# Kernel tuning notes

Hardware: AMD Instinct MI355X
Metric: run time of the kernel (lower is better)

Reference implementation:

```python
import jax, jax.numpy as jnp
import numpy as np

T, H, I, E, TOPK = 4096, 2880, 2880, 16, 4
EPS = 1e-5
ALPHA = 1.702


def setup_inputs() -> dict:
    key = jax.random.key(0)
    ks = jax.random.split(key, 8)
    s = 0.02
    return {
        "x": jax.random.normal(ks[0], (T, H), dtype=jnp.float32),
        "norm_w": jnp.ones((H,), dtype=jnp.float32),
        "gate_w": jax.random.normal(ks[1], (E, H), dtype=jnp.float32) * s,
        "gate_b": jax.random.normal(ks[2], (E,), dtype=jnp.float32) * s,
        "w1": jax.random.normal(ks[3], (E, 2 * I, H), dtype=jnp.float32) * s,  # fused gate_up
        "b1": jax.random.normal(ks[4], (E, 2 * I), dtype=jnp.float32) * s,
        "w2": jax.random.normal(ks[5], (E, H, I), dtype=jnp.float32) * s,      # down proj
        "b2": jax.random.normal(ks[6], (E, H), dtype=jnp.float32) * s,
    }


def _rmsnorm(x, w, eps=EPS):
    var = jnp.mean(x * x, axis=-1, keepdims=True)
    return x * jax.lax.rsqrt(var + eps) * w


def _swiglu(gu):
    glu, lin = jnp.split(gu, 2, axis=-1)
    return glu * jax.nn.sigmoid(ALPHA * glu) * (lin + 1.0)


def reference(x, norm_w, gate_w, gate_b, w1, b1, w2, b2):
    t = _rmsnorm(x, norm_w)                       # [T, H]
    logits = t @ gate_w.T + gate_b                # [T, E]
    # Renormalize routing: top-k of logits, softmax over the k selected logits
    vals, idx = jax.lax.top_k(logits, TOPK)       # [T, k]
    wts = jax.nn.softmax(vals, axis=-1)           # [T, k]
    combine = jnp.zeros((t.shape[0], E), dtype=t.dtype)
    combine = combine.at[jnp.arange(t.shape[0])[:, None], idx].set(wts)  # [T, E]
    out = jnp.zeros_like(x)
    for e in range(E):                            # small fixed expert loop
        gu = t @ w1[e].T + b1[e]                  # [T, 2I]
        y = _swiglu(gu) @ w2[e].T + b2[e]         # [T, H]
        out = out + combine[:, e:e + 1] * y
    return x + out
```

## Files before the change

kernel.cpp:

```cpp
#include <hip/hip_runtime.h>
#include <hip/hip_bf16.h>
#include <math.h>
#include <stdint.h>

#define T_TOK 4096
#define H_DIM 2880
#define E_NUM 16
#define ALPHA 1.702f
#define EPS_RMS 1e-5f

#define PADM 192
#define BK 32
#define NK (H_DIM / BK)
#define MAX_RT 104
#define NCT1 30
#define NCT2 15
#define G1 (MAX_RT * NCT1)
#define G2 (MAX_RT * NCT2)
#define ABUF 12288
#define BBUF 12288
#define BOFF 36864

typedef __attribute__((ext_vector_type(8))) short short8;
typedef __attribute__((ext_vector_type(4))) float f32x4;

__device__ __forceinline__ unsigned short f2bf(float f) {
  unsigned u = __float_as_uint(f);
  return (unsigned short)((u + 0x7fffu + ((u >> 16) & 1u)) >> 16);
}
__device__ __forceinline__ unsigned cpk(float a, float b) {
  unsigned r;
  asm("v_cvt_pk_bf16_f32 %0, %1, %2" : "=v"(r) : "v"(a), "v"(b));
  return r;
}
__device__ __forceinline__ void gl_lds16(const void* g, unsigned char* lds_dst) {
  __builtin_amdgcn_global_load_lds(
      (const __attribute__((address_space(1))) void*)g,
      (__attribute__((address_space(3))) void*)lds_dst, 16, 0, 0);
}
#define ENDSTEP() do {                                           \
    asm volatile("s_waitcnt lgkmcnt(0)" ::: "memory");           \
    __builtin_amdgcn_s_barrier();                                \
    __builtin_amdgcn_sched_barrier(0);                           \
  } while (0)

__global__ __launch_bounds__(256) void k_norm_gate(
    const float* __restrict__ x, const float* __restrict__ norm_w,
    const float* __restrict__ gate_w, const float* __restrict__ gate_b,
    unsigned short* __restrict__ t_out,
    int* __restrict__ topk_id, float* __restrict__ topk_w,
    int* __restrict__ counts)
{
  int t = blockIdx.x, tid = threadIdx.x;
  const float4* xr = (const float4*)(x + (size_t)t * H_DIM);
  float4 xa[3];
  float ss = 0.f;
  int j = 0;
  for (int i = tid; i < 720; i += 256, j++) {
    float4 v = xr[i]; xa[j] = v;
    ss += v.x * v.x + v.y * v.y + v.z * v.z + v.w * v.w;
  }
#pragma unroll
  for (int o = 1; o < 64; o <<= 1) ss += __shfl_xor(ss, o, 64);
  __shared__ float red[4];
  if ((tid & 63) == 0) red[tid >> 6] = ss;
  __syncthreads();
  float rs = rsqrtf((red[0] + red[1] + red[2] + red[3]) * (1.f / H_DIM) + EPS_RMS);

  float part[16];
#pragma unroll
  for (int q = 0; q < 16; q++) part[q] = 0.f;
  j = 0;
  for (int i = tid; i < 720; i += 256, j++) {
    float4 v = xa[j];
    float4 w = ((const float4*)norm_w)[i];
    float t0 = v.x * rs * w.x, t1 = v.y * rs * w.y;
    float t2 = v.z * rs * w.z, t3 = v.w * rs * w.w;
    ushort4 b; b.x = f2bf(t0); b.y = f2bf(t1); b.z = f2bf(t2); b.w = f2bf(t3);
    ((ushort4*)(t_out + (size_t)t * H_DIM))[i] = b;
#pragma unroll
    for (int q = 0; q < 16; q++) {
      float4 g = ((const float4*)(gate_w + (size_t)q * H_DIM))[i];
      part[q] += t0 * g.x + t1 * g.y + t2 * g.z + t3 * g.w;
    }
  }
  __shared__ float lg[4][16];
#pragma unroll
  for (int q = 0; q < 16; q++) {
    float p = part[q];
#pragma unroll
    for (int o = 1; o < 64; o <<= 1) p += __shfl_xor(p, o, 64);
    if ((tid & 63) == 0) lg[tid >> 6][q] = p;
  }
  __syncthreads();
  if (tid == 0) {
    float logit[16];
    for (int q = 0; q < 16; q++)
      logit[q] = lg[0][q] + lg[1][q] + lg[2][q] + lg[3][q] + gate_b[q];
    unsigned used = 0; int idx[4]; float val[4];
    for (int k = 0; k < 4; k++) {
      float best = -3.4e38f; int bi = 0;
      for (int q = 0; q < 16; q++)
        if (!((used >> q) & 1u) && logit[q] > best) { best = logit[q]; bi = q; }
      used |= 1u << bi; idx[k] = bi; val[k] = best;
    }
    float s0 = 0.f, w4[4];
    for (int k = 0; k < 4; k++) { w4[k] = expf(val[k] - val[0]); s0 += w4[k]; }
    for (int k = 0; k < 4; k++) {
      topk_id[t * 4 + k] = idx[k];
      topk_w[t * 4 + k] = w4[k] / s0;
      atomicAdd(&counts[idx[k]], 1);
    }
  }
}

__global__ void k_offsets(const int* __restrict__ counts, int* __restrict__ d_off) {
  if (threadIdx.x == 0) {
    int acc = 0;
    for (int q = 0; q < 16; q++) {
      d_off[q] = acc;
      acc += ((counts[q] + PADM - 1) / PADM) * PADM;
    }
    d_off[16] = acc;
  }
}

__global__ __launch_bounds__(256) void k_fill(
    const int* __restrict__ topk_id, const float* __restrict__ topk_w,
    const int* __restrict__ counts, const int* __restrict__ d_off,
    int* __restrict__ perm_tok, float* __restrict__ perm_w,
    int* __restrict__ perm_sl)
{
  int e = blockIdx.x;
  int base = d_off[e], pe = d_off[e + 1] - base, cnt = counts[e];
  int tid = threadIdx.x, lane = tid & 63, wv = tid >> 6;
  __shared__ int wsum[4];
  int pos = 0;
  for (int c0 = 0; c0 < T_TOK; c0 += 256) {
    int tok = c0 + tid;
    int4 ids = ((const int4*)topk_id)[tok];
    int flag = 0, slot = 0;
    if (ids.x == e) { flag = 1; slot = 0; }
    else if (ids.y == e) { flag = 1; slot = 1; }
    else if (ids.z == e) { flag = 1; slot = 2; }
    else if (ids.w == e) { flag = 1; slot = 3; }
    unsigned long long b = __ballot(flag);
    int wprefix = __popcll(b & ((1ULL << lane) - 1ULL));
    if (lane == 0) wsum[wv] = __popcll(b);
    __syncthreads();
    int woff = 0;
    for (int i = 0; i < wv; i++) woff += wsum[i];
    int tot = wsum[0] + wsum[1] + wsum[2] + wsum[3];
    if (flag) {
      int p = base + pos + woff + wprefix;
      perm_tok[p] = tok;
      perm_w[p] = topk_w[tok * 4 + slot];
      perm_sl[p] = slot;
    }
    pos += tot;
    __syncthreads();
  }
  for (int i = cnt + tid; i < pe; i += 256) {
    perm_tok[base + i] = -1;
    perm_w[base + i] = 0.f;
    perm_sl[base + i] = 0;
  }
}

#define STAGE_A(abuf, ktn) do {                                               \
  gl_lds16(aptr0 + (size_t)(ktn) * BK, lds + (abuf) * ABUF + adst0);          \
  if (tid < 256)                                                              \
    gl_lds16(aptr1 + (size_t)(ktn) * BK, lds + (abuf) * ABUF + adst1);        \
} while (0)

#define LOAD_B(ktn) do {                                                      \
  bv[0][0] = bptr0[(ktn) * 8]; bv[0][1] = bptr0[(ktn) * 8 + 1];               \
  if (tid < 256) { bv[1][0] = bptr1[(ktn) * 8]; bv[1][1] = bptr1[(ktn) * 8 + 1]; } \
} while (0)

#define PACK_B(bbuf) do {                                                     \
  uint4 p0;                                                                   \
  p0.x = cpk(bv[0][0].x, bv[0][0].y); p0.y = cpk(bv[0][0].z, bv[0][0].w);     \
  p0.z = cpk(bv[0][1].x, bv[0][1].y); p0.w = cpk(bv[0][1].z, bv[0][1].w);     \
  *(uint4*)(lds + BOFF + (bbuf) * BBUF + bdst0) = p0;                         \
  if (tid < 256) {                                                            \
    uint4 p1;                                                                 \
    p1.x = cpk(bv[1][0].x, bv[1][0].y); p1.y = cpk(bv[1][0].z, bv[1][0].w);   \
    p1.z = cpk(bv[1][1].x, bv[1][1].y); p1.w = cpk(bv[1][1].z, bv[1][1].w);   \
    *(uint4*)(lds + BOFF + (bbuf) * BBUF + bdst1) = p1;                       \
  }                                                                           \
} while (0)

#define GEMM_PIPE(COMP) do {                                                  \
  STAGE_A(0, 0); STAGE_A(1, 1); LOAD_B(0);                                    \
  PACK_B(0);                                                                  \
  ENDSTEP();                                                                  \
  int ca = 0;                                                                 \
  _Pragma("unroll 1")                                                         \
  for (int u = 0; u < NK / 2; u++) {                                          \
    int kt = 2 * u;                                                           \
    int ca1 = ca + 1; if (ca1 >= 3) ca1 -= 3;                                 \
    int ca2 = ca + 2; if (ca2 >= 3) ca2 -= 3;                                 \
    if (kt + 1 < NK) LOAD_B(kt + 1);                                          \
    if (kt + 2 < NK) STAGE_A(ca2, kt + 2);                                    \
    COMP(ca, 0);                                                              \
    if (kt + 1 < NK) PACK_B(1);                                               \
    ENDSTEP();                                                                \
    if (kt + 2 < NK) LOAD_B(kt + 2);                                          \
    if (kt + 3 < NK) STAGE_A(ca, kt + 3);                                     \
    COMP(ca1, 1);                                                             \
    if (kt + 2 < NK) PACK_B(0);                                               \
    ENDSTEP();                                                                \
    ca = ca2;                                                                 \
  }                                                                           \
} while (0)

#define COMP1(ab, bb) do {                                                    \
  const unsigned char* Ab = lds + (ab) * ABUF;                                \
  const unsigned char* Bb = lds + BOFF + (bb) * BBUF;                         \
  short8 a0 = *(const short8*)(Ab + abase);                                   \
  short8 a1 = *(const short8*)(Ab + abase + 1024);                            \
  short8 a2 = *(const short8*)(Ab + abase + 2048);                            \
  __builtin_amdgcn_s_setprio(1);                                              \
  _Pragma("unroll")                                                           \
  for (int n = 0; n < 3; n++) {                                               \
    short8 bg = *(const short8*)(Bb + bgbase + n * 1024);                     \
    short8 bl = *(const short8*)(Bb + blbase + n * 1024);                     \
    accg[0][n] = __builtin_amdgcn_mfma_f32_16x16x32_bf16(a0, bg, accg[0][n], 0, 0, 0); \
    accg[1][n] = __builtin_amdgcn_mfma_f32_16x16x32_bf16(a1, bg, accg[1][n], 0, 0, 0); \
    accg[2][n] = __builtin_amdgcn_mfma_f32_16x16x32_bf16(a2, bg, accg[2][n], 0, 0, 0); \
    accl[0][n] = __builtin_amdgcn_mfma_f32_16x16x32_bf16(a0, bl, accl[0][n], 0, 0, 0); \
    accl[1][n] = __builtin_amdgcn_mfma_f32_16x16x32_bf16(a1, bl, accl[1][n], 0, 0, 0); \
    accl[2][n] = __builtin_amdgcn_mfma_f32_16x16x32_bf16(a2, bl, accl[2][n], 0, 0, 0); \
  }                                                                           \
  __builtin_amdgcn_s_setprio(0);                                              \
} while (0)

#define COMP2(ab, bb) do {                                                    \
  const unsigned char* Ab = lds + (ab) * ABUF;                                \
  const unsigned char* Bb = lds + BOFF + (bb) * BBUF;                         \
  short8 a0 = *(const short8*)(Ab + abase);                                   \
  short8 a1 = *(const short8*)(Ab + abase + 1024);                            \
  short8 a2 = *(const short8*)(Ab + abase + 2048);                            \
  __builtin_amdgcn_s_setprio(1);                                              \
  _Pragma("unroll")                                                           \
  for (int n = 0; n < 6; n++) {                                               \
    short8 b = *(const short8*)(Bb + bbase + n * 1024);                       \
    acc[0][n] = __builtin_amdgcn_mfma_f32_16x16x32_bf16(a0, b, acc[0][n], 0, 0, 0); \
    acc[1][n] = __builtin_amdgcn_mfma_f32_16x16x32_bf16(a1, b, acc[1][n], 0, 0, 0); \
    acc[2][n] = __builtin_amdgcn_mfma_f32_16x16x32_bf16(a2, b, acc[2][n], 0, 0, 0); \
  }                                                                           \
  __builtin_amdgcn_s_setprio(0);                                              \
} while (0)

__global__ __launch_bounds__(512, 4) void k_gemm1(
    const unsigned short* __restrict__ t_bf16,
    const float* __restrict__ w1, const float* __restrict__ b1,
    const int* __restrict__ perm_tok, const int* __restrict__ d_off,
    unsigned short* __restrict__ act)
{
  __shared__ __align__(16) unsigned char lds[3 * ABUF + 2 * BBUF];
  const int total = d_off[16];
  int bid = blockIdx.x;
  int wg = (bid & 7) * (G1 / 8) + (bid >> 3);
  int ct = wg / MAX_RT, rt = wg % MAX_RT;
  int rowbase = rt * PADM;
  if (rowbase >= total) return;
  int e = 0;
#pragma unroll
  for (int q = 0; q < E_NUM; q++) if (d_off[q + 1] <= rowbase) e = q + 1;

  int tid = threadIdx.x, lane = tid & 63, wv = tid >> 6;
  int wm = wv & 3, wn = wv >> 2;
  int lr = lane & 15, ch = lane >> 4;
  unsigned swz16 = (unsigned)((ch ^ ((lr >> 1) & 3)) << 4);
  unsigned abase  = (unsigned)((wm * 48 + lr) * 64) + swz16;
  unsigned bgbase = (unsigned)((wn * 48 + lr) * 64) + swz16;
  unsigned blbase = bgbase + 6144;

  const unsigned short* aptr0; const unsigned short* aptr1 = 0;
  unsigned adst0, adst1 = 0;
  {
    int cl = tid, r = cl >> 2, c = cl & 3;
    int tok = perm_tok[rowbase + r]; if (tok < 0) tok = 0;
    aptr0 = t_bf16 + (size_t)tok * H_DIM + ((c ^ ((r >> 1) & 3)) * 8);
    adst0 = (unsigned)cl * 16;
  }
  if (tid < 256) {
    int cl = 512 + tid, r = cl >> 2, c = cl & 3;
    int tok = perm_tok[rowbase + r]; if (tok < 0) tok = 0;
    aptr1 = t_bf16 + (size_t)tok * H_DIM + ((c ^ ((r >> 1) & 3)) * 8);
    adst1 = (unsigned)cl * 16;
  }
  const float4* bptr0; const float4* bptr1 = 0;
  unsigned bdst0, bdst1 = 0;
  {
    int cl = tid, rr = cl >> 2, c = cl & 3;
    size_t grow = (size_t)e * (2 * H_DIM) +
                  (rr < 96 ? (size_t)(ct * 96 + rr) : (size_t)(H_DIM + ct * 96 + (rr - 96)));
    bptr0 = (const float4*)(w1 + grow * H_DIM) + c * 2;
    bdst0 = (unsigned)(rr * 64 + ((c ^ ((rr >> 1) & 3)) << 4));
  }
  if (tid < 256) {
    int cl = 512 + tid, rr = cl >> 2, c = cl & 3;
    size_t grow = (size_t)(H_DIM + ct * 96 + (rr - 96)) + (size_t)e * (2 * H_DIM);
    bptr1 = (const float4*)(w1 + grow * H_DIM) + c * 2;
    bdst1 = (unsigned)(rr * 64 + ((c ^ ((rr >> 1) & 3)) << 4));
  }

  f32x4 zero = {0.f, 0.f, 0.f, 0.f};
  f32x4 accg[3][3], accl[3][3];
#pragma unroll
  for (int m = 0; m < 3; m++)
#pragma unroll
    for (int n = 0; n < 3; n++) { accg[m][n] = zero; accl[m][n] = zero; }
  float4 bv[2][2];

  GEMM_PIPE(COMP1);

  int rq = lane >> 4;
#pragma unroll
  for (int m = 0; m < 3; m++) {
    int row0 = rowbase + wm * 48 + m * 16 + rq * 4;
#pragma unroll
    for (int n = 0; n < 3; n++) {
      int col = ct * 96 + wn * 48 + n * 16 + lr;
      float bg = b1[(size_t)e * (2 * H_DIM) + col];
      float bl = b1[(size_t)e * (2 * H_DIM) + H_DIM + col];
#pragma unroll
      for (int j = 0; j < 4; j++) {
        float g = accg[m][n][j] + bg;
        float l = accl[m][n][j] + bl;
        float s = 1.f / (1.f + __expf(-ALPHA * g));
        act[(size_t)(row0 + j) * H_DIM + col] = f2bf(g * s * (l + 1.f));
      }
    }
  }
}

__global__ __launch_bounds__(512, 4) void k_gemm2(
    const unsigned short* __restrict__ act,
    const float* __restrict__ w2, const float* __restrict__ b2,
    const int* __restrict__ perm_tok, const float* __restrict__ perm_w,
    const int* __restrict__ perm_sl, const int* __restrict__ d_off,
    unsigned short* __restrict__ yslot)
{
  __shared__ __align__(16) unsigned char lds[3 * ABUF + 2 * BBUF];
  __shared__ int stok[PADM]; __shared__ float swt[PADM]; __shared__ int ssl[PADM];
  const int total = d_off[16];
  int bid = blockIdx.x;
  int wg = (bid & 7) * (G2 / 8) + (bid >> 3);
  int ct = wg / MAX_RT, rt = wg % MAX_RT;
  int rowbase = rt * PADM;
  if (rowbase >= total) return;
  int e = 0;
#pragma unroll
  for (int q = 0; q < E_NUM; q++) if (d_off[q + 1] <= rowbase) e = q + 1;

  int tid = threadIdx.x, lane = tid & 63, wv = tid >> 6;
  int wm = wv & 3, wn = wv >> 2;
  int lr = lane & 15, ch = lane >> 4;
  unsigned swz16 = (unsigned)((ch ^ ((lr >> 1) & 3)) << 4);
  unsigned abase = (unsigned)((wm * 48 + lr) * 64) + swz16;
  unsigned bbase = (unsigned)((wn * 96 + lr) * 64) + swz16;

  if (tid < PADM) {
    stok[tid] = perm_tok[rowbase + tid];
    swt[tid] = perm_w[rowbase + tid];
    ssl[tid] = perm_sl[rowbase + tid];
  }

  const unsigned short* aptr0; const unsigned short* aptr1 = 0;
  unsigned adst0, adst1 = 0;
  {
    int cl = tid, r = cl >> 2, c = cl & 3;
    aptr0 = act + (size_t)(rowbase + r) * H_DIM + ((c ^ ((r >> 1) & 3)) * 8);
    adst0 = (unsigned)cl * 16;
  }
  if (tid < 256) {
    int cl = 512 + tid, r = cl >> 2, c = cl & 3;
    aptr1 = act + (size_t)(rowbase + r) * H_DIM + ((c ^ ((r >> 1) & 3)) * 8);
    adst1 = (unsigned)cl * 16;
  }
  const float4* bptr0; const float4* bptr1 = 0;
  unsigned bdst0, bdst1 = 0;
  {
    int cl = tid, rr = cl >> 2, c = cl & 3;
    size_t grow = (size_t)e * H_DIM + (size_t)(ct * 192 + rr);
    bptr0 = (const float4*)(w2 + grow * H_DIM) + c * 2;
    bdst0 = (unsigned)(rr * 64 + ((c ^ ((rr >> 1) & 3)) << 4));
  }
  if (tid < 256) {
    int cl = 512 + tid, rr = cl >> 2, c = cl & 3;
    size_t grow = (size_t)e * H_DIM + (size_t)(ct * 192 + rr);
    bptr1 = (const float4*)(w2 + grow * H_DIM) + c * 2;
    bdst1 = (unsigned)(rr * 64 + ((c ^ ((rr >> 1) & 3)) << 4));
  }

  f32x4 zero = {0.f, 0.f, 0.f, 0.f};
  f32x4 acc[3][6];
#pragma unroll
  for (int m = 0; m < 3; m++)
#pragma unroll
    for (int n = 0; n < 6; n++) acc[m][n] = zero;
  float4 bv[2][2];

  GEMM_PIPE(COMP2);

  int rq = lane >> 4;
#pragma unroll
  for (int m = 0; m < 3; m++) {
    int rl0 = wm * 48 + m * 16 + rq * 4;
#pragma unroll
    for (int n = 0; n < 6; n++) {
      int col = ct * 192 + wn * 96 + n * 16 + lr;
      float b2v = b2[(size_t)e * H_DIM + col];
#pragma unroll
      for (int j = 0; j < 4; j++) {
        int rl = rl0 + j;
        int tk = stok[rl];
        if (tk >= 0) {
          float y = (acc[m][n][j] + b2v) * swt[rl];
          yslot[((size_t)ssl[rl] * T_TOK + tk) * H_DIM + col] = f2bf(y);
        }
      }
    }
  }
}

__global__ __launch_bounds__(256) void k_comb(
    const float* __restrict__ x, const unsigned short* __restrict__ yslot,
    float* __restrict__ out)
{
  const int n8 = T_TOK * H_DIM / 8;
  int i = blockIdx.x * 256 + threadIdx.x;
  int stride = gridDim.x * 256;
  for (; i < n8; i += stride) {
    float4 x0 = ((const float4*)x)[2 * i];
    float4 x1 = ((const float4*)x)[2 * i + 1];
    float s[8] = {x0.x, x0.y, x0.z, x0.w, x1.x, x1.y, x1.z, x1.w};
#pragma unroll
    for (int k = 0; k < 4; k++) {
      uint4 v = ((const uint4*)(yslot + (size_t)k * T_TOK * H_DIM))[i];
      unsigned u[4] = {v.x, v.y, v.z, v.w};
#pragma unroll
      for (int q = 0; q < 4; q++) {
        s[2 * q]     += __uint_as_float(u[q] << 16);
        s[2 * q + 1] += __uint_as_float(u[q] & 0xffff0000u);
      }
    }
    float4 o0 = {s[0], s[1], s[2], s[3]};
    float4 o1 = {s[4], s[5], s[6], s[7]};
    ((float4*)out)[2 * i] = o0;
    ((float4*)out)[2 * i + 1] = o1;
  }
}

extern "C" void kernel_launch(void* const* d_in, const int* in_sizes, int n_in,
                              void* d_out, int out_size, void* d_ws, size_t ws_size,
                              hipStream_t stream)
{
  const float* x      = (const float*)d_in[0];
  const float* norm_w = (const float*)d_in[1];
  const float* gate_w = (const float*)d_in[2];
  const float* gate_b = (const float*)d_in[3];
  const float* w1     = (const float*)d_in[4];
  const float* b1     = (const float*)d_in[5];
  const float* w2     = (const float*)d_in[6];
  const float* b2     = (const float*)d_in[7];
  float* out = (float*)d_out;
  char* ws = (char*)d_ws;

  unsigned short* t_bf16  = (unsigned short*)(ws);
  unsigned short* act     = (unsigned short*)(ws + 23592960);
  int*            topk_id = (int*)(ws + 138608640);
  float*          topk_w  = (float*)(ws + 138674176);
  int*            perm_tk = (int*)(ws + 138739712);
  float*          perm_w  = (float*)(ws + 138819584);
  int*            perm_sl = (int*)(ws + 138899456);
  int*            counts  = (int*)(ws + 138979328);
  int*            d_off   = (int*)(ws + 138979392);
  unsigned short* yslot   = (unsigned short*)(ws + 138979840);

  hipMemsetAsync(counts, 0, 64, stream);
  hipLaunchKernelGGL(k_norm_gate, dim3(T_TOK), dim3(256), 0, stream,
                     x, norm_w, gate_w, gate_b, t_bf16, topk_id, topk_w, counts);
  hipLaunchKernelGGL(k_offsets, dim3(1), dim3(64), 0, stream, counts, d_off);
  hipLaunchKernelGGL(k_fill, dim3(16), dim3(256), 0, stream,
                     topk_id, topk_w, counts, d_off, perm_tk, perm_w, perm_sl);
  hipLaunchKernelGGL(k_gemm1, dim3(G1), dim3(512), 0, stream,
                     t_bf16, w1, b1, perm_tk, d_off, act);
  hipLaunchKernelGGL(k_gemm2, dim3(G2), dim3(512), 0, stream,
                     act, w2, b2, perm_tk, perm_w, perm_sl, d_off, yslot);
  hipLaunchKernelGGL(k_comb, dim3(2048), dim3(256), 0, stream, x, yslot, out);
}
```

Before: 1.484 ms.

## Load A fragments directly from global into registers, drop A LDS staging

```diff
diff --git a/kernel.cpp b/kernel.cpp
--- a/kernel.cpp
+++ b/kernel.cpp
@@ -17,9 +17,7 @@
 #define NCT2 15
 #define G1 (MAX_RT * NCT1)
 #define G2 (MAX_RT * NCT2)
-#define ABUF 12288
 #define BBUF 12288
-#define BOFF 36864
 
 typedef __attribute__((ext_vector_type(8))) short short8;
 typedef __attribute__((ext_vector_type(4))) float f32x4;
@@ -32,11 +30,6 @@
   unsigned r;
   asm("v_cvt_pk_bf16_f32 %0, %1, %2" : "=v"(r) : "v"(a), "v"(b));
   return r;
-}
-__device__ __forceinline__ void gl_lds16(const void* g, unsigned char* lds_dst) {
-  __builtin_amdgcn_global_load_lds(
-      (const __attribute__((address_space(1))) void*)g,
-      (__attribute__((address_space(3))) void*)lds_dst, 16, 0, 0);
 }
 #define ENDSTEP() do {                                           \
     asm volatile("s_waitcnt lgkmcnt(0)" ::: "memory");           \
@@ -167,10 +160,10 @@
   }
 }
 
-#define STAGE_A(abuf, ktn) do {                                               \
-  gl_lds16(aptr0 + (size_t)(ktn) * BK, lds + (abuf) * ABUF + adst0);          \
-  if (tid < 256)                                                              \
-    gl_lds16(aptr1 + (size_t)(ktn) * BK, lds + (abuf) * ABUF + adst1);        \
+#define LOAD_A(ar, ktn) do {                                                  \
+  ar[0] = *(const short8*)(aptrs[0] + (size_t)(ktn) * 64);                    \
+  ar[1] = *(const short8*)(aptrs[1] + (size_t)(ktn) * 64);                    \
+  ar[2] = *(const short8*)(aptrs[2] + (size_t)(ktn) * 64);                    \
 } while (0)
 
 #define LOAD_B(ktn) do {                                                      \
@@ -182,84 +175,71 @@
   uint4 p0;                                                                   \
   p0.x = cpk(bv[0][0].x, bv[0][0].y); p0.y = cpk(bv[0][0].z, bv[0][0].w);     \
   p0.z = cpk(bv[0][1].x, bv[0][1].y); p0.w = cpk(bv[0][1].z, bv[0][1].w);     \
-  *(uint4*)(lds + BOFF + (bbuf) * BBUF + bdst0) = p0;                         \
+  *(uint4*)(lds + (bbuf) * BBUF + bdst0) = p0;                                \
   if (tid < 256) {                                                            \
     uint4 p1;                                                                 \
     p1.x = cpk(bv[1][0].x, bv[1][0].y); p1.y = cpk(bv[1][0].z, bv[1][0].w);   \
     p1.z = cpk(bv[1][1].x, bv[1][1].y); p1.w = cpk(bv[1][1].z, bv[1][1].w);   \
-    *(uint4*)(lds + BOFF + (bbuf) * BBUF + bdst1) = p1;                       \
+    *(uint4*)(lds + (bbuf) * BBUF + bdst1) = p1;                              \
   }                                                                           \
 } while (0)
 
 #define GEMM_PIPE(COMP) do {                                                  \
-  STAGE_A(0, 0); STAGE_A(1, 1); LOAD_B(0);                                    \
+  LOAD_A(arA, 0);                                                             \
+  LOAD_B(0);                                                                  \
   PACK_B(0);                                                                  \
   ENDSTEP();                                                                  \
-  int ca = 0;                                                                 \
   _Pragma("unroll 1")                                                         \
   for (int u = 0; u < NK / 2; u++) {                                          \
     int kt = 2 * u;                                                           \
-    int ca1 = ca + 1; if (ca1 >= 3) ca1 -= 3;                                 \
-    int ca2 = ca + 2; if (ca2 >= 3) ca2 -= 3;                                 \
-    if (kt + 1 < NK) LOAD_B(kt + 1);                                          \
-    if (kt + 2 < NK) STAGE_A(ca2, kt + 2);                                    \
-    COMP(ca, 0);                                                              \
+    if (kt + 1 < NK) { LOAD_B(kt + 1); LOAD_A(arB, kt + 1); }                 \
+    COMP(arA, 0);                                                             \
     if (kt + 1 < NK) PACK_B(1);                                               \
     ENDSTEP();                                                                \
-    if (kt + 2 < NK) LOAD_B(kt + 2);                                          \
-    if (kt + 3 < NK) STAGE_A(ca, kt + 3);                                     \
-    COMP(ca1, 1);                                                             \
+    if (kt + 2 < NK) { LOAD_B(kt + 2); LOAD_A(arA, kt + 2); }                 \
+    COMP(arB, 1);                                                             \
     if (kt + 2 < NK) PACK_B(0);                                               \
     ENDSTEP();                                                                \
-    ca = ca2;                                                                 \
   }                                                                           \
 } while (0)
 
-#define COMP1(ab, bb) do {                                                    \
-  const unsigned char* Ab = lds + (ab) * ABUF;                                \
-  const unsigned char* Bb = lds + BOFF + (bb) * BBUF;                         \
-  short8 a0 = *(const short8*)(Ab + abase);                                   \
-  short8 a1 = *(const short8*)(Ab + abase + 1024);                            \
-  short8 a2 = *(const short8*)(Ab + abase + 2048);                            \
+#define COMP1(ar, bb) do {                                                    \
+  const unsigned char* Bb = lds + (bb) * BBUF;                                \
   __builtin_amdgcn_s_setprio(1);                                              \
   _Pragma("unroll")                                                           \
   for (int n = 0; n < 3; n++) {                                               \
     short8 bg = *(const short8*)(Bb + bgbase + n * 1024);                     \
     short8 bl = *(const short8*)(Bb + blbase + n * 1024);                     \
-    accg[0][n] = __builtin_amdgcn_mfma_f32_16x16x32_bf16(a0, bg, accg[0][n], 0, 0, 0); \
-    accg[1][n] = __builtin_amdgcn_mfma_f32_16x16x32_bf16(a1, bg, accg[1][n], 0, 0, 0); \
-    accg[2][n] = __builtin_amdgcn_mfma_f32_16x16x32_bf16(a2, bg, accg[2][n], 0, 0, 0); \
-    accl[0][n] = __builtin_amdgcn_mfma_f32_16x16x32_bf16(a0, bl, accl[0][n], 0, 0, 0); \
-    accl[1][n] = __builtin_amdgcn_mfma_f32_16x16x32_bf16(a1, bl, accl[1][n], 0, 0, 0); \
-    accl[2][n] = __builtin_amdgcn_mfma_f32_16x16x32_bf16(a2, bl, accl[2][n], 0, 0, 0); \
+    accg[0][n] = __builtin_amdgcn_mfma_f32_16x16x32_bf16(ar[0], bg, accg[0][n], 0, 0, 0); \
+    accg[1][n] = __builtin_amdgcn_mfma_f32_16x16x32_bf16(ar[1], bg, accg[1][n], 0, 0, 0); \
+    accg[2][n] = __builtin_amdgcn_mfma_f32_16x16x32_bf16(ar[2], bg, accg[2][n], 0, 0, 0); \
+    accl[0][n] = __builtin_amdgcn_mfma_f32_16x16x32_bf16(ar[0], bl, accl[0][n], 0, 0, 0); \
+    accl[1][n] = __builtin_amdgcn_mfma_f32_16x16x32_bf16(ar[1], bl, accl[1][n], 0, 0, 0); \
+    accl[2][n] = __builtin_amdgcn_mfma_f32_16x16x32_bf16(ar[2], bl, accl[2][n], 0, 0, 0); \
   }                                                                           \
   __builtin_amdgcn_s_setprio(0);                                              \
 } while (0)
 
-#define COMP2(ab, bb) do {                                                    \
-  const unsigned char* Ab = lds + (ab) * ABUF;                                \
-  const unsigned char* Bb = lds + BOFF + (bb) * BBUF;                         \
-  short8 a0 = *(const short8*)(Ab + abase);                                   \
-  short8 a1 = *(const short8*)(Ab + abase + 1024);                            \
-  short8 a2 = *(const short8*)(Ab + abase + 2048);                            \
+#define COMP2(ar, bb) do {                                                    \
+  const unsigned char* Bb = lds + (bb) * BBUF;                                \
   __builtin_amdgcn_s_setprio(1);                                              \
   _Pragma("unroll")                                                           \
   for (int n = 0; n < 6; n++) {                                               \
     short8 b = *(const short8*)(Bb + bbase + n * 1024);                       \
-    acc[0][n] = __builtin_amdgcn_mfma_f32_16x16x32_bf16(a0, b, acc[0][n], 0, 0, 0); \
-    acc[1][n] = __builtin_amdgcn_mfma_f32_16x16x32_bf16(a1, b, acc[1][n], 0, 0, 0); \
-    acc[2][n] = __builtin_amdgcn_mfma_f32_16x16x32_bf16(a2, b, acc[2][n], 0, 0, 0); \
+    acc[0][n] = __builtin_amdgcn_mfma_f32_16x16x32_bf16(ar[0], b, acc[0][n], 0, 0, 0); \
+    acc[1][n] = __builtin_amdgcn_mfma_f32_16x16x32_bf16(ar[1], b, acc[1][n], 0, 0, 0); \
+    acc[2][n] = __builtin_amdgcn_mfma_f32_16x16x32_bf16(ar[2], b, acc[2][n], 0, 0, 0); \
   }                                                                           \
   __builtin_amdgcn_s_setprio(0);                                              \
 } while (0)
 
-__global__ __launch_bounds__(512, 4) void k_gemm1(
+__global__ __launch_bounds__(512, 2) void k_gemm1(
     const unsigned short* __restrict__ t_bf16,
     const float* __restrict__ w1, const float* __restrict__ b1,
     const int* __restrict__ perm_tok, const int* __restrict__ d_off,
     unsigned short* __restrict__ act)
 {
-  __shared__ __align__(16) unsigned char lds[3 * ABUF + 2 * BBUF];
+  __shared__ __align__(16) unsigned char lds[2 * BBUF];
   const int total = d_off[16];
   int bid = blockIdx.x;
   int wg = (bid & 7) * (G1 / 8) + (bid >> 3);
@@ -274,23 +254,15 @@
   int wm = wv & 3, wn = wv >> 2;
   int lr = lane & 15, ch = lane >> 4;
   unsigned swz16 = (unsigned)((ch ^ ((lr >> 1) & 3)) << 4);
-  unsigned abase  = (unsigned)((wm * 48 + lr) * 64) + swz16;
   unsigned bgbase = (unsigned)((wn * 48 + lr) * 64) + swz16;
   unsigned blbase = bgbase + 6144;
 
-  const unsigned short* aptr0; const unsigned short* aptr1 = 0;
-  unsigned adst0, adst1 = 0;
-  {
-    int cl = tid, r = cl >> 2, c = cl & 3;
-    int tok = perm_tok[rowbase + r]; if (tok < 0) tok = 0;
-    aptr0 = t_bf16 + (size_t)tok * H_DIM + ((c ^ ((r >> 1) & 3)) * 8);
-    adst0 = (unsigned)cl * 16;
-  }
-  if (tid < 256) {
-    int cl = 512 + tid, r = cl >> 2, c = cl & 3;
-    int tok = perm_tok[rowbase + r]; if (tok < 0) tok = 0;
-    aptr1 = t_bf16 + (size_t)tok * H_DIM + ((c ^ ((r >> 1) & 3)) * 8);
-    adst1 = (unsigned)cl * 16;
+  const unsigned char* aptrs[3];
+#pragma unroll
+  for (int f = 0; f < 3; f++) {
+    int row = rowbase + wm * 48 + f * 16 + lr;
+    int tok = perm_tok[row]; if (tok < 0) tok = 0;
+    aptrs[f] = (const unsigned char*)(t_bf16 + (size_t)tok * H_DIM) + ch * 16;
   }
   const float4* bptr0; const float4* bptr1 = 0;
   unsigned bdst0, bdst1 = 0;
@@ -315,6 +287,7 @@
 #pragma unroll
     for (int n = 0; n < 3; n++) { accg[m][n] = zero; accl[m][n] = zero; }
   float4 bv[2][2];
+  short8 arA[3], arB[3];
 
   GEMM_PIPE(COMP1);
 
@@ -338,14 +311,14 @@
   }
 }
 
-__global__ __launch_bounds__(512, 4) void k_gemm2(
+__global__ __launch_bounds__(512, 2) void k_gemm2(
     const unsigned short* __restrict__ act,
     const float* __restrict__ w2, const float* __restrict__ b2,
     const int* __restrict__ perm_tok, const float* __restrict__ perm_w,
     const int* __restrict__ perm_sl, const int* __restrict__ d_off,
     unsigned short* __restrict__ yslot)
 {
-  __shared__ __align__(16) unsigned char lds[3 * ABUF + 2 * BBUF];
+  __shared__ __align__(16) unsigned char lds[2 * BBUF];
   __shared__ int stok[PADM]; __shared__ float swt[PADM]; __shared__ int ssl[PADM];
   const int total = d_off[16];
   int bid = blockIdx.x;
@@ -361,7 +334,6 @@
   int wm = wv & 3, wn = wv >> 2;
   int lr = lane & 15, ch = lane >> 4;
   unsigned swz16 = (unsigned)((ch ^ ((lr >> 1) & 3)) << 4);
-  unsigned abase = (unsigned)((wm * 48 + lr) * 64) + swz16;
   unsigned bbase = (unsigned)((wn * 96 + lr) * 64) + swz16;
 
   if (tid < PADM) {
@@ -370,17 +342,11 @@
     ssl[tid] = perm_sl[rowbase + tid];
   }
 
-  const unsigned short* aptr0; const unsigned short* aptr1 = 0;
-  unsigned adst0, adst1 = 0;
-  {
-    int cl = tid, r = cl >> 2, c = cl & 3;
-    aptr0 = act + (size_t)(rowbase + r) * H_DIM + ((c ^ ((r >> 1) & 3)) * 8);
-    adst0 = (unsigned)cl * 16;
-  }
-  if (tid < 256) {
-    int cl = 512 + tid, r = cl >> 2, c = cl & 3;
-    aptr1 = act + (size_t)(rowbase + r) * H_DIM + ((c ^ ((r >> 1) & 3)) * 8);
-    adst1 = (unsigned)cl * 16;
+  const unsigned char* aptrs[3];
+#pragma unroll
+  for (int f = 0; f < 3; f++) {
+    int row = rowbase + wm * 48 + f * 16 + lr;
+    aptrs[f] = (const unsigned char*)(act + (size_t)row * H_DIM) + ch * 16;
   }
   const float4* bptr0; const float4* bptr1 = 0;
   unsigned bdst0, bdst1 = 0;
@@ -404,6 +370,7 @@
 #pragma unroll
     for (int n = 0; n < 6; n++) acc[m][n] = zero;
   float4 bv[2][2];
+  short8 arA[3], arB[3];
 
   GEMM_PIPE(COMP2);
 
```

New measurement: 2.436 ms. +64.1%, slower.
